# Performance work log

Measured on AMD Instinct MI355X. Metric: run time of the kernel, lower is better.

Reference implementation:

```python
import jax, jax.numpy as jnp
import numpy as np

CONF_THRESH = 0.05      # confidence_threshold
IOU_THRESH = 0.15       # nms_iou_threshold
MAX_PER_CLASS = 550     # max_detection_per_class
MAX_TOTAL = 1100        # max_detection
NEG = -1e9              # sentinel for suppressed / below-threshold scores


def _to_corners(b):
    # convert_to_min_max_corner: (cx, cy, w, h) -> (x1, y1, x2, y2)
    xy, wh = b[..., :2], b[..., 2:4]
    return jnp.concatenate([xy - wh * 0.5, xy + wh * 0.5], axis=-1)


def _area(b):
    return jnp.clip(b[..., 2] - b[..., 0], 0.0) * jnp.clip(b[..., 3] - b[..., 1], 0.0)


def _iou_one_many(box, boxes):
    # box: [4], boxes: [N,4] in corner format
    lt = jnp.maximum(box[:2], boxes[:, :2])
    rb = jnp.minimum(box[2:], boxes[:, 2:])
    wh = jnp.clip(rb - lt, 0.0)
    inter = wh[:, 0] * wh[:, 1]
    union = _area(box) + _area(boxes) - inter
    return inter / jnp.maximum(union, 1e-8)


def _nms_single(boxes, scores):
    # Exact greedy hard-NMS for one (image, class): boxes [N,4], scores [N]
    s0 = jnp.where(scores > CONF_THRESH, scores, NEG)

    def step(s, _):
        i = jnp.argmax(s)
        sc = s[i]
        suppress = _iou_one_many(boxes[i], boxes) > IOU_THRESH
        ns = jnp.where(suppress, NEG, s).at[i].set(NEG)
        return ns, (i, sc)

    _, (sel_idx, sel_score) = jax.lax.scan(step, s0, None, length=MAX_PER_CLASS)
    return sel_idx, sel_score  # [K], [K]


def _decode(predictions):
    boxes = _to_corners(predictions[:, :, :4])          # [B,N,4]
    cls_probs = jax.nn.sigmoid(predictions[:, :, 4:])   # [B,N,C]
    scores = jnp.transpose(cls_probs, (0, 2, 1))        # [B,C,N]

    nms = jax.vmap(jax.vmap(_nms_single, in_axes=(None, 0)), in_axes=(0, 0))
    sel_idx, sel_score = nms(boxes, scores)             # [B,C,K]
    B, C, K = sel_score.shape

    gboxes = jnp.take_along_axis(boxes[:, None, :, :], sel_idx[..., None], axis=2)  # [B,C,K,4]
    classes = jnp.broadcast_to(jnp.arange(C, dtype=jnp.float32)[None, :, None], (B, C, K))

    fb = gboxes.reshape(B, C * K, 4)
    fs = sel_score.reshape(B, C * K)
    fc = classes.reshape(B, C * K)

    k = min(MAX_TOTAL, C * K)
    top_s, top_i = jax.lax.top_k(fs, k)                 # combined cross-class top-k
    tb = jnp.take_along_axis(fb, top_i[..., None], axis=1)
    tc = jnp.take_along_axis(fc, top_i, axis=1)

    valid = top_s > 0.5 * NEG                           # real detections have score in (conf, 1]
    nmsed_boxes = jnp.where(valid[..., None], tb, 0.0)
    nmsed_scores = jnp.where(valid, top_s, 0.0)
    nmsed_classes = jnp.where(valid, tc, 0.0)
    valid_detections = jnp.sum(valid, axis=1).astype(jnp.int32)
    return nmsed_boxes, nmsed_scores, nmsed_classes, valid_detections


def setup_inputs() -> dict:
    key = jax.random.key(0)
    k1, k2, k3 = jax.random.split(key, 3)
    B, N, C, IMG = 4, 49104, 2, 512.0
    u = jax.random.uniform(k1, (B, N, 4), dtype=jnp.float32)
    cxcy = u[..., :2] * IMG                  # centers within the image
    wh = 16.0 + u[..., 2:] * 128.0           # plausible anchor-ish sizes
    logits = jax.random.normal(k2, (B, N, C), dtype=jnp.float32) * 1.5 - 3.0
    predictions = jnp.concatenate([cxcy, wh, logits], axis=-1)  # [B,N,6]
    images = jax.random.uniform(k3, (B, 512, 512, 3), dtype=jnp.float32)
    return {"images": images, "predictions": predictions}


def reference(images, predictions):
    # images is accepted (as in the Keras layer) but unused by the math
    return _decode(predictions)
```

## Files before the change

kernel.cpp:

```cpp
#include <hip/hip_runtime.h>
#include <stdint.h>

#define NEGV    (-1000000000.0f)
#define CONF    0.05f
#define MAXSEL  550
#define CAP     32768
#define HEAD    1024
#define HW      (HEAD / 64)
#define NBINS   4096
#define BINBASE 0xC07F0000u
#define GCAP    3072
#define NSEG    64
#define TROUNDS 3

typedef unsigned long long u64;
typedef unsigned int u32;

__device__ __forceinline__ float areaf(float4 b) {
    return __fmul_rn(fmaxf(__fsub_rn(b.z, b.x), 0.0f), fmaxf(__fsub_rn(b.w, b.y), 0.0f));
}

__device__ __forceinline__ bool iou_gt2(float4 a, float aA, float4 b, float aB) {
    float ltx = fmaxf(a.x, b.x), lty = fmaxf(a.y, b.y);
    float rbx = fminf(a.z, b.z), rby = fminf(a.w, b.w);
    float wx = fmaxf(__fsub_rn(rbx, ltx), 0.0f);
    float wy = fmaxf(__fsub_rn(rby, lty), 0.0f);
    float inter = __fmul_rn(wx, wy);
    float uni = fmaxf(__fsub_rn(__fadd_rn(aA, aB), inter), 1e-8f);
    const double M = (double)0.15f + 0x1p-27;
    return (double)inter > M * (double)uni;
}

__device__ __forceinline__ u32 binof(u32 keyhi) {
    u32 bin = (keyhi - BINBASE) >> 14;
    return bin > (NBINS - 1) ? (NBINS - 1) : bin;
}

__global__ void k_decode(const float* __restrict__ pred, float4* __restrict__ boxes,
                         u32* __restrict__ hist, u32* __restrict__ llen,
                         u32* __restrict__ S_arr, u32* __restrict__ Sold,
                         int BN, int NBC) {
    int t = blockIdx.x * 256 + threadIdx.x;
    if (t < 2 * NBC * NBINS) hist[t] = 0;
    if (t < 2 * NBC) llen[t] = 0;
    if (t < NBC) { S_arr[t] = 0; Sold[t] = 0; }
    if (t >= BN) return;
    const float* p = pred + (size_t)t * 6;
    float cx = p[0], cy = p[1], w = p[2], h = p[3];
    float hw = __fmul_rn(w, 0.5f), hh = __fmul_rn(h, 0.5f);
    float4 b;
    b.x = __fsub_rn(cx, hw);
    b.y = __fsub_rn(cy, hh);
    b.z = __fadd_rn(cx, hw);
    b.w = __fadd_rn(cy, hh);
    boxes[t] = b;
}

__global__ __launch_bounds__(256) void k_hist(const float* __restrict__ pred,
                                              u32* __restrict__ hist,
                                              u64* __restrict__ L0,
                                              u32* __restrict__ llen0,
                                              int Nn, int Cc, int TIL) {
    int bt = blockIdx.x;
    int tile = bt % TIL, bc = bt / TIL;
    int b = bc / Cc, c = bc % Cc;
    int n = tile * 256 + threadIdx.x;
    bool p = false; u32 hi = 0;
    if (n < Nn) {
        float lg = pred[((size_t)b * Nn + n) * 6 + 4 + c];
        float sc = __fdiv_rn(1.0f, __fadd_rn(1.0f, expf(-lg)));
        if (sc > CONF) {
            p = true;
            hi = ~__float_as_uint(sc);
            atomicAdd(&hist[bc * NBINS + binof(hi)], 1u);
        }
    }
    u64 bal = __ballot(p);
    __shared__ u32 wb[4]; __shared__ u32 base;
    int lane = threadIdx.x & 63, wv = threadIdx.x >> 6;
    if (lane == 0) wb[wv] = (u32)__popcll(bal);
    __syncthreads();
    if (threadIdx.x == 0) {
        u32 run = 0;
        for (int q = 0; q < 4; ++q) { u32 v = wb[q]; wb[q] = run; run += v; }
        base = run ? atomicAdd(&llen0[bc], run) : 0u;
    }
    __syncthreads();
    if (p) {
        u32 pos = base + wb[wv] + (u32)__popcll(bal & ((1ull << lane) - 1ull));
        if (pos < CAP)
            L0[(size_t)bc * CAP + pos] = ((u64)hi << 32) | (u32)n;
    }
}

__global__ __launch_bounds__(1024) void k_headsort(const u64* __restrict__ list,
                                                   const u32* __restrict__ llen_cur,
                                                   const u32* __restrict__ hc,
                                                   u32* __restrict__ hn,
                                                   u32* __restrict__ ln,
                                                   const float4* __restrict__ boxes,
                                                   const u32* __restrict__ S_arr,
                                                   u64* __restrict__ headkey,
                                                   float4* __restrict__ headbox,
                                                   float* __restrict__ headarea,
                                                   u32* __restrict__ hl_arr,
                                                   u64* __restrict__ hmax_arr,
                                                   int Nn, int Cc) {
    int bc = blockIdx.x, b = bc / Cc;
    int tid = threadIdx.x, lane = tid & 63, wv = tid >> 6;
    __shared__ u64 buf[4096];
    __shared__ u32 gcnt;
    __shared__ int s_t;
    for (int i = tid; i < NBINS; i += 1024) hn[bc * NBINS + i] = 0;
    if (tid == 0) { ln[bc] = 0; gcnt = 0; }
    __syncthreads();
    if ((int)S_arr[bc] >= MAXSEL) { if (tid == 0) hl_arr[bc] = 0; return; }
    int len = (int)llen_cur[bc]; if (len > CAP) len = CAP;
    if (wv == 0) {
        if (lane == 0) s_t = -1;
        const u32* h = hc + bc * NBINS;
        int base = lane * 64;
        u32 s = 0;
        for (int i = 0; i < 64; ++i) s += h[base + i];
        u32 p = s;
        for (int d = 1; d < 64; d <<= 1) { u32 o = __shfl_up(p, d); if (lane >= d) p += o; }
        u32 total = __shfl(p, 63);
        u32 K = total < HEAD ? total : HEAD;
        if (K > 0) {
            u64 bal = __ballot(p >= K);
            int tl = (int)__builtin_ctzll(bal);
            if (lane == tl) {
                u32 cum = p - s;
                for (int i = 0; i < 64; ++i) {
                    cum += h[base + i];
                    if (cum >= K) {
                        s_t = (cum <= GCAP) ? (base + i) : (base + i - 1);
                        break;
                    }
                }
            }
        }
    }
    __syncthreads();
    int t = s_t;
    if (t >= 0) {
        const u64* src = list + (size_t)bc * CAP;
        for (int i = tid; i < len; i += 1024) {
            u64 key = src[i];
            if ((int)binof((u32)(key >> 32)) <= t) {
                u32 pos = atomicAdd(&gcnt, 1u);
                if (pos < GCAP) buf[pos] = key;
            }
        }
    }
    __syncthreads();
    int g = (int)gcnt; if (g > GCAP) g = GCAP;
    int SN = 1; while (SN < g) SN <<= 1;
    for (int i = g + tid; i < SN; i += 1024) buf[i] = ~0ull;
    __syncthreads();
    for (int k = 2; k <= SN; k <<= 1) {
        for (int j = k >> 1; j > 0; j >>= 1) {
            for (int idx = tid; idx < SN / 2; idx += 1024) {
                int i = ((idx & ~(j - 1)) << 1) | (idx & (j - 1));
                int q = i | j;
                bool up = ((i & k) == 0);
                u64 x = buf[i], y = buf[q];
                if ((x > y) == up) { buf[i] = y; buf[q] = x; }
            }
            __syncthreads();
        }
    }
    int hl = g < HEAD ? g : HEAD;
    if (tid == 0) { hl_arr[bc] = (u32)hl; hmax_arr[bc] = hl > 0 ? buf[hl - 1] : 0ull; }
    for (int i = tid; i < hl; i += 1024) {
        u64 key = buf[i];
        headkey[bc * HEAD + i] = key;
        float4 bx = boxes[(size_t)b * Nn + (u32)key];
        headbox[bc * HEAD + i] = bx;
        headarea[bc * HEAD + i] = areaf(bx);
    }
}

__global__ __launch_bounds__(256) void k_premask(const float4* __restrict__ headbox,
                                                 const float* __restrict__ headarea,
                                                 const u32* __restrict__ hl_arr,
                                                 u64* __restrict__ masks) {
    int blk = blockIdx.x, bc = blk >> 4, rb = blk & 15;
    int hl = (int)hl_arr[bc];
    if (hl <= 0) return;
    __shared__ float4 chB[HEAD];
    __shared__ float  chA[HEAD];
    for (int i = threadIdx.x; i < hl; i += 256) {
        chB[i] = headbox[bc * HEAD + i];
        chA[i] = headarea[bc * HEAD + i];
    }
    __syncthreads();
    int r = (rb << 6) + (threadIdx.x & 63);
    int part = threadIdx.x >> 6;
    if (r >= hl) return;
    float4 a = chB[r]; float aA = chA[r];
    u64* row = masks + ((size_t)bc * HEAD + r) * HW;
    for (int w = part * 4; w < part * 4 + 4; ++w) {
        u64 bits = 0;
        int cb = w << 6;
        int j1 = hl - cb; if (j1 > 64) j1 = 64;
        int j0 = (cb > r) ? 0 : (r + 1 - cb);
        for (int j = j0; j < j1; ++j)
            if (iou_gt2(a, aA, chB[cb + j], chA[cb + j])) bits |= (1ull << j);
        row[w] = bits;
    }
}

__global__ __launch_bounds__(1024) void k_chain(const u64* __restrict__ headkey,
                                                const u32* __restrict__ hl_arr,
                                                const u64* __restrict__ masks,
                                                const float4* __restrict__ headbox,
                                                const float* __restrict__ headarea,
                                                u32* __restrict__ sel_n,
                                                float* __restrict__ sel_s,
                                                float4* __restrict__ selb_g,
                                                float* __restrict__ sela_g,
                                                u32* __restrict__ S_arr,
                                                u32* __restrict__ Sold) {
    int bc = blockIdx.x;
    int tid = threadIdx.x, lane = tid & 63;
    __shared__ u64 mrow[HEAD * HW];
    __shared__ u64 kky[HEAD];
    __shared__ u32 selidx[MAXSEL];
    __shared__ int s_S;
    int S0 = (int)S_arr[bc];
    if (tid == 0) Sold[bc] = (u32)S0;
    int hl = (int)hl_arr[bc];
    if (hl <= 0 || S0 >= MAXSEL) return;
    const u64* gm = masks + (size_t)bc * HEAD * HW;
    for (int i = tid; i < hl * HW; i += 1024) mrow[i] = gm[i];
    for (int i = tid; i < hl; i += 1024) kky[i] = headkey[bc * HEAD + i];
    __syncthreads();
    if (tid < 64) {
        u64 rem = ~0ull;
        if (lane < HW) {
            int lo = lane << 6;
            rem = (hl >= lo + 64) ? 0ull : (hl <= lo ? ~0ull : ~((1ull << (hl - lo)) - 1ull));
        }
        int S = S0;
        while (S < MAXSEL) {
            bool av = (lane < HW) && (rem != ~0ull);
            u64 bal = __ballot(av);
            if (!bal) break;
            int w0 = (int)__builtin_ctzll(bal);
            u64 nz = __shfl((u64)(~rem), w0);
            int kz = (int)__builtin_ctzll(nz);
            int i = (w0 << 6) + kz;
            if (lane == 0) selidx[S] = (u32)i;
            if (lane < HW) rem |= mrow[i * HW + lane];
            if (lane == w0) rem |= (1ull << kz);
            ++S;
        }
        if (lane == 0) { s_S = S; S_arr[bc] = (u32)S; }
    }
    __syncthreads();
    int S = s_S;
    for (int s = S0 + tid; s < S; s += 1024) {
        u32 i = selidx[s];
        u64 k64 = kky[i];
        sel_n[bc * MAXSEL + s] = (u32)k64;
        sel_s[bc * MAXSEL + s] = __uint_as_float(~(u32)(k64 >> 32));
        selb_g[bc * MAXSEL + s] = headbox[bc * HEAD + i];
        sela_g[bc * MAXSEL + s] = headarea[bc * HEAD + i];
    }
}

__global__ __launch_bounds__(256) void k_mark(const float4* __restrict__ boxes,
                                              const u64* __restrict__ Lc,
                                              const u32* __restrict__ llen_c,
                                              const float4* __restrict__ selb_g,
                                              const float* __restrict__ sela_g,
                                              const u32* __restrict__ S_arr,
                                              const u32* __restrict__ Sold,
                                              const u64* __restrict__ hmax_arr,
                                              const u32* __restrict__ hl_arr,
                                              u64* __restrict__ Ln,
                                              u32* __restrict__ llen_n,
                                              u32* __restrict__ hist_n,
                                              int Nn, int Cc) {
    int blk = blockIdx.x, bc = blk / NSEG, seg = blk % NSEG;
    int tid = threadIdx.x, lane = tid & 63, wv = tid >> 6;
    int b = bc / Cc;
    int S0 = (int)Sold[bc], S1 = (int)S_arr[bc];
    if (S1 >= MAXSEL) return;
    int len = (int)llen_c[bc]; if (len > CAP) len = CAP;
    if (len <= 0) return;
    int ns = S1 - S0;
    u64 hmax = ((int)hl_arr[bc] > 0) ? hmax_arr[bc] : 0ull;
    __shared__ float4 sb[MAXSEL];
    __shared__ float  sa[MAXSEL];
    for (int s = tid; s < ns; s += 256) {
        sb[s] = selb_g[bc * MAXSEL + S0 + s];
        sa[s] = sela_g[bc * MAXSEL + S0 + s];
    }
    __syncthreads();
    __shared__ u32 wb[4]; __shared__ u32 base;
    int chunk = (len + NSEG - 1) / NSEG;
    int lo = seg * chunk, hi2 = lo + chunk; if (hi2 > len) hi2 = len;
    const u64* src = Lc + (size_t)bc * CAP;
    u64* dst = Ln + (size_t)bc * CAP;
    for (int st = lo; st < hi2; st += 256) {
        int i = st + tid;
        bool alive = i < hi2; u64 key = 0;
        if (alive) {
            key = src[i];
            if (key <= hmax) alive = false;
            else {
                float4 bx = boxes[(size_t)b * Nn + (u32)key];
                float aA = areaf(bx);
                for (int s = 0; s < ns; ++s)
                    if (iou_gt2(bx, aA, sb[s], sa[s])) { alive = false; break; }
            }
        }
        u64 bal = __ballot(alive);
        if (lane == 0) wb[wv] = (u32)__popcll(bal);
        __syncthreads();
        if (tid == 0) {
            u32 run = 0;
            for (int q = 0; q < 4; ++q) { u32 v = wb[q]; wb[q] = run; run += v; }
            base = run ? atomicAdd(&llen_n[bc], run) : 0u;
        }
        __syncthreads();
        if (alive) {
            u32 pos = base + wb[wv] + (u32)__popcll(bal & ((1ull << lane) - 1ull));
            if (pos < CAP) dst[pos] = key;
            atomicAdd(&hist_n[bc * NBINS + binof((u32)(key >> 32))], 1u);
        }
        __syncthreads();
    }
}

__global__ __launch_bounds__(1024) void k_final(const u32* __restrict__ selcnt,
                                                const u32* __restrict__ sel_n,
                                                const float* __restrict__ sel_s,
                                                const float4* __restrict__ boxes,
                                                float* __restrict__ out,
                                                int Nn, int Cc, int Bb) {
    int b = blockIdx.x, tid = threadIdx.x;
    const int TOT = MAXSEL * 2;
    __shared__ u64 sk[2048];
    u32 c0 = selcnt[b * Cc + 0];
    u32 c1 = selcnt[b * Cc + 1];
    for (int t = tid; t < 2048; t += 1024) {
        u64 key;
        if (t < TOT) {
            int c = t / MAXSEL, k2 = t % MAXSEL;
            u32 cc = (c == 0) ? c0 : c1;
            float sc = (k2 < (int)cc) ? sel_s[(size_t)(b * Cc + c) * MAXSEL + k2] : NEGV;
            u32 u = __float_as_uint(sc);
            u32 ord = (u & 0x80000000u) ? ~u : (u | 0x80000000u);
            key = (((u64)(~ord)) << 32) | (u32)t;
        } else {
            key = ~0ull;
        }
        sk[t] = key;
    }
    __syncthreads();
    for (int k = 2; k <= 2048; k <<= 1) {
        for (int j = k >> 1; j > 0; j >>= 1) {
            int idx = tid;
            int i = ((idx & ~(j - 1)) << 1) | (idx & (j - 1));
            int p = i | j;
            bool up = ((i & k) == 0);
            u64 x = sk[i], y = sk[p];
            if ((x > y) == up) { sk[i] = y; sk[p] = x; }
            __syncthreads();
        }
    }
    int off_scores = Bb * TOT * 4;
    int off_classes = off_scores + Bb * TOT;
    int off_valid = off_classes + Bb * TOT;
    for (int r = tid; r < TOT; r += 1024) {
        u64 key = sk[r];
        u32 flat = (u32)(key & 0xffffffffull);
        u32 hi = (u32)(key >> 32);
        u32 ord = ~hi;
        float sc = (ord & 0x80000000u) ? __uint_as_float(ord & 0x7fffffffu)
                                       : __uint_as_float(~ord);
        bool valid = sc > -5.0e8f;
        int c = (int)(flat / MAXSEL), k2 = (int)(flat % MAXSEL);
        float4 bxv = make_float4(0.f, 0.f, 0.f, 0.f);
        float so = 0.f, co = 0.f;
        if (valid) {
            u32 n = sel_n[(size_t)(b * Cc + c) * MAXSEL + k2];
            bxv = boxes[(size_t)b * Nn + n];
            so = sc;
            co = (float)c;
        }
        ((float4*)out)[b * TOT + r] = bxv;
        out[off_scores + b * TOT + r] = so;
        out[off_classes + b * TOT + r] = co;
    }
    if (tid == 0) out[off_valid + b] = (float)(c0 + c1);
}

extern "C" void kernel_launch(void* const* d_in, const int* in_sizes, int n_in,
                              void* d_out, int out_size, void* d_ws, size_t ws_size,
                              hipStream_t stream) {
    const float* pred = (const float*)d_in[1];
    float* out = (float*)d_out;
    int Bb = out_size / 6601;
    int Nn = in_sizes[1] / (6 * Bb);
    const int Cc = 2;
    if (Bb <= 0 || Nn <= 0) return;
    int NBC = Bb * Cc;
    int TIL = (Nn + 255) / 256;

    char* ws = (char*)d_ws;
    size_t off = 0;
    auto alloc = [&](size_t bytes) { void* p = ws + off; off = (off + bytes + 255) & ~(size_t)255; return p; };
    float4* boxes   = (float4*)alloc((size_t)Bb * Nn * 16);
    u64* L0         = (u64*)alloc((size_t)NBC * CAP * 8);
    u64* L1         = (u64*)alloc((size_t)NBC * CAP * 8);
    u32* hist       = (u32*)alloc(2 * (size_t)NBC * NBINS * 4);
    u32* llen       = (u32*)alloc(2 * NBC * 4);
    u64* headkey    = (u64*)alloc((size_t)NBC * HEAD * 8);
    float4* headbox = (float4*)alloc((size_t)NBC * HEAD * 16);
    float* headarea = (float*)alloc((size_t)NBC * HEAD * 4);
    u32* hl_arr     = (u32*)alloc(NBC * 4);
    u64* hmax_arr   = (u64*)alloc(NBC * 8);
    u32* sel_n      = (u32*)alloc((size_t)NBC * MAXSEL * 4);
    float* sel_s    = (float*)alloc((size_t)NBC * MAXSEL * 4);
    float4* selb_g  = (float4*)alloc((size_t)NBC * MAXSEL * 16);
    float* sela_g   = (float*)alloc((size_t)NBC * MAXSEL * 4);
    u32* S_arr      = (u32*)alloc(NBC * 4);
    u32* Sold       = (u32*)alloc(NBC * 4);
    u64* masks      = (u64*)alloc((size_t)NBC * HEAD * HW * 8);
    if (off > ws_size) return;

    int BN = Bb * Nn;
    k_decode<<<(BN + 255) / 256, 256, 0, stream>>>(pred, boxes, hist, llen, S_arr, Sold, BN, NBC);
    k_hist<<<NBC * TIL, 256, 0, stream>>>(pred, hist, L0, llen, Nn, Cc, TIL);

    for (int r = 0; r < TROUNDS; ++r) {
        int cur = r & 1, nxt = (r + 1) & 1;
        u64* Lc = cur ? L1 : L0;
        u64* Ln = nxt ? L1 : L0;
        u32* lc = llen + cur * NBC;
        u32* ln = llen + nxt * NBC;
        u32* hc = hist + (size_t)cur * NBC * NBINS;
        u32* hn = hist + (size_t)nxt * NBC * NBINS;
        k_headsort<<<NBC, 1024, 0, stream>>>(Lc, lc, hc, hn, ln, boxes, S_arr,
                                             headkey, headbox, headarea, hl_arr, hmax_arr, Nn, Cc);
        k_premask<<<NBC * 16, 256, 0, stream>>>(headbox, headarea, hl_arr, masks);
        k_chain<<<NBC, 1024, 0, stream>>>(headkey, hl_arr, masks, headbox, headarea,
                                          sel_n, sel_s, selb_g, sela_g, S_arr, Sold);
        if (r + 1 < TROUNDS)
            k_mark<<<NBC * NSEG, 256, 0, stream>>>(boxes, Lc, lc, selb_g, sela_g, S_arr, Sold,
                                                   hmax_arr, hl_arr, Ln, ln, hn, Nn, Cc);
    }
    k_final<<<Bb, 1024, 0, stream>>>(S_arr, sel_n, sel_s, boxes, out, Nn, Cc, Bb);
}
```

Before: 359.2 us.

## Fuse decode with histogram build and fold IoU mask into headsort

Merges the box-decode and per-class histogram/list-building kernels into one pass that reads each prediction row once and handles both classes. Zeroing of hist/llen/S counters moves to a single memset, and the separate premask kernel is folded into headsort, so each thread computes its whole mask row from shared memory. This cuts the launch count per round and avoids rereading head boxes from global memory. The trade-off is that the mask computation now runs on only NBC blocks instead of NBC*16, which lowers parallelism, and headsort uses more shared memory.

```diff
diff --git a/kernel.cpp b/kernel.cpp
--- a/kernel.cpp
+++ b/kernel.cpp
@@ -36,60 +36,60 @@
     return bin > (NBINS - 1) ? (NBINS - 1) : bin;
 }
 
-__global__ void k_decode(const float* __restrict__ pred, float4* __restrict__ boxes,
-                         u32* __restrict__ hist, u32* __restrict__ llen,
-                         u32* __restrict__ S_arr, u32* __restrict__ Sold,
-                         int BN, int NBC) {
-    int t = blockIdx.x * 256 + threadIdx.x;
-    if (t < 2 * NBC * NBINS) hist[t] = 0;
-    if (t < 2 * NBC) llen[t] = 0;
-    if (t < NBC) { S_arr[t] = 0; Sold[t] = 0; }
-    if (t >= BN) return;
-    const float* p = pred + (size_t)t * 6;
-    float cx = p[0], cy = p[1], w = p[2], h = p[3];
-    float hw = __fmul_rn(w, 0.5f), hh = __fmul_rn(h, 0.5f);
-    float4 b;
-    b.x = __fsub_rn(cx, hw);
-    b.y = __fsub_rn(cy, hh);
-    b.z = __fadd_rn(cx, hw);
-    b.w = __fadd_rn(cy, hh);
-    boxes[t] = b;
-}
-
-__global__ __launch_bounds__(256) void k_hist(const float* __restrict__ pred,
-                                              u32* __restrict__ hist,
-                                              u64* __restrict__ L0,
-                                              u32* __restrict__ llen0,
-                                              int Nn, int Cc, int TIL) {
-    int bt = blockIdx.x;
-    int tile = bt % TIL, bc = bt / TIL;
-    int b = bc / Cc, c = bc % Cc;
-    int n = tile * 256 + threadIdx.x;
-    bool p = false; u32 hi = 0;
-    if (n < Nn) {
-        float lg = pred[((size_t)b * Nn + n) * 6 + 4 + c];
-        float sc = __fdiv_rn(1.0f, __fadd_rn(1.0f, expf(-lg)));
-        if (sc > CONF) {
-            p = true;
-            hi = ~__float_as_uint(sc);
-            atomicAdd(&hist[bc * NBINS + binof(hi)], 1u);
-        }
-    }
-    u64 bal = __ballot(p);
-    __shared__ u32 wb[4]; __shared__ u32 base;
-    int lane = threadIdx.x & 63, wv = threadIdx.x >> 6;
-    if (lane == 0) wb[wv] = (u32)__popcll(bal);
-    __syncthreads();
-    if (threadIdx.x == 0) {
-        u32 run = 0;
-        for (int q = 0; q < 4; ++q) { u32 v = wb[q]; wb[q] = run; run += v; }
-        base = run ? atomicAdd(&llen0[bc], run) : 0u;
-    }
-    __syncthreads();
-    if (p) {
-        u32 pos = base + wb[wv] + (u32)__popcll(bal & ((1ull << lane) - 1ull));
-        if (pos < CAP)
-            L0[(size_t)bc * CAP + pos] = ((u64)hi << 32) | (u32)n;
+__global__ __launch_bounds__(256) void k_build(const float* __restrict__ pred,
+                                               float4* __restrict__ boxes,
+                                               u32* __restrict__ hist,
+                                               u64* __restrict__ L0,
+                                               u32* __restrict__ llen0,
+                                               int Nn, int Cc, int TIL) {
+    int blk = blockIdx.x;
+    int tile = blk % TIL, b = blk / TIL;
+    int tid = threadIdx.x, lane = tid & 63, wv = tid >> 6;
+    int n = tile * 256 + tid;
+    bool inb = n < Nn;
+    float lg0 = 0.f, lg1 = 0.f;
+    if (inb) {
+        size_t base = ((size_t)b * Nn + n) * 6;
+        const float2* pp = (const float2*)(pred + base);
+        float2 r0 = pp[0], r1 = pp[1], r2 = pp[2];
+        float cx = r0.x, cy = r0.y, w = r1.x, h = r1.y;
+        float hw = __fmul_rn(w, 0.5f), hh = __fmul_rn(h, 0.5f);
+        float4 bx;
+        bx.x = __fsub_rn(cx, hw);
+        bx.y = __fsub_rn(cy, hh);
+        bx.z = __fadd_rn(cx, hw);
+        bx.w = __fadd_rn(cy, hh);
+        boxes[(size_t)b * Nn + n] = bx;
+        lg0 = r2.x; lg1 = r2.y;
+    }
+    __shared__ u32 wb[4]; __shared__ u32 sbase;
+    for (int c = 0; c < Cc; ++c) {
+        int bc = b * Cc + c;
+        bool p = false; u32 hi = 0;
+        if (inb) {
+            float lg = (c == 0) ? lg0 : lg1;
+            float sc = __fdiv_rn(1.0f, __fadd_rn(1.0f, expf(-lg)));
+            if (sc > CONF) {
+                p = true;
+                hi = ~__float_as_uint(sc);
+                atomicAdd(&hist[bc * NBINS + binof(hi)], 1u);
+            }
+        }
+        u64 bal = __ballot(p);
+        if (lane == 0) wb[wv] = (u32)__popcll(bal);
+        __syncthreads();
+        if (tid == 0) {
+            u32 run = 0;
+            for (int q = 0; q < 4; ++q) { u32 v = wb[q]; wb[q] = run; run += v; }
+            sbase = run ? atomicAdd(&llen0[bc], run) : 0u;
+        }
+        __syncthreads();
+        if (p) {
+            u32 pos = sbase + wb[wv] + (u32)__popcll(bal & ((1ull << lane) - 1ull));
+            if (pos < CAP)
+                L0[(size_t)bc * CAP + pos] = ((u64)hi << 32) | (u32)n;
+        }
+        __syncthreads();
     }
 }
 
@@ -105,10 +105,13 @@
                                                    float* __restrict__ headarea,
                                                    u32* __restrict__ hl_arr,
                                                    u64* __restrict__ hmax_arr,
+                                                   u64* __restrict__ masks,
                                                    int Nn, int Cc) {
     int bc = blockIdx.x, b = bc / Cc;
     int tid = threadIdx.x, lane = tid & 63, wv = tid >> 6;
     __shared__ u64 buf[4096];
+    __shared__ float4 chB[HEAD];
+    __shared__ float  chA[HEAD];
     __shared__ u32 gcnt;
     __shared__ int s_t;
     for (int i = tid; i < NBINS; i += 1024) hn[bc * NBINS + i] = 0;
@@ -178,36 +181,22 @@
         float4 bx = boxes[(size_t)b * Nn + (u32)key];
         headbox[bc * HEAD + i] = bx;
         headarea[bc * HEAD + i] = areaf(bx);
-    }
-}
-
-__global__ __launch_bounds__(256) void k_premask(const float4* __restrict__ headbox,
-                                                 const float* __restrict__ headarea,
-                                                 const u32* __restrict__ hl_arr,
-                                                 u64* __restrict__ masks) {
-    int blk = blockIdx.x, bc = blk >> 4, rb = blk & 15;
-    int hl = (int)hl_arr[bc];
-    if (hl <= 0) return;
-    __shared__ float4 chB[HEAD];
-    __shared__ float  chA[HEAD];
-    for (int i = threadIdx.x; i < hl; i += 256) {
-        chB[i] = headbox[bc * HEAD + i];
-        chA[i] = headarea[bc * HEAD + i];
-    }
-    __syncthreads();
-    int r = (rb << 6) + (threadIdx.x & 63);
-    int part = threadIdx.x >> 6;
-    if (r >= hl) return;
-    float4 a = chB[r]; float aA = chA[r];
-    u64* row = masks + ((size_t)bc * HEAD + r) * HW;
-    for (int w = part * 4; w < part * 4 + 4; ++w) {
-        u64 bits = 0;
-        int cb = w << 6;
-        int j1 = hl - cb; if (j1 > 64) j1 = 64;
-        int j0 = (cb > r) ? 0 : (r + 1 - cb);
-        for (int j = j0; j < j1; ++j)
-            if (iou_gt2(a, aA, chB[cb + j], chA[cb + j])) bits |= (1ull << j);
-        row[w] = bits;
+        chB[i] = bx;
+        chA[i] = areaf(bx);
+    }
+    __syncthreads();
+    if (tid < hl) {
+        float4 a = chB[tid]; float aA = chA[tid];
+        u64* row = masks + ((size_t)bc * HEAD + tid) * HW;
+        for (int w = 0; w < HW; ++w) {
+            u64 bits = 0;
+            int cb = w << 6;
+            int j1 = hl - cb; if (j1 > 64) j1 = 64;
+            int j0 = (cb > tid) ? 0 : (tid + 1 - cb);
+            for (int j = j0; j < j1; ++j)
+                if (iou_gt2(a, aA, chB[cb + j], chA[cb + j])) bits |= (1ull << j);
+            row[w] = bits;
+        }
     }
 }
 
@@ -417,8 +406,6 @@
     float4* boxes   = (float4*)alloc((size_t)Bb * Nn * 16);
     u64* L0         = (u64*)alloc((size_t)NBC * CAP * 8);
     u64* L1         = (u64*)alloc((size_t)NBC * CAP * 8);
-    u32* hist       = (u32*)alloc(2 * (size_t)NBC * NBINS * 4);
-    u32* llen       = (u32*)alloc(2 * NBC * 4);
     u64* headkey    = (u64*)alloc((size_t)NBC * HEAD * 8);
     float4* headbox = (float4*)alloc((size_t)NBC * HEAD * 16);
     float* headarea = (float*)alloc((size_t)NBC * HEAD * 4);
@@ -428,14 +415,17 @@
     float* sel_s    = (float*)alloc((size_t)NBC * MAXSEL * 4);
     float4* selb_g  = (float4*)alloc((size_t)NBC * MAXSEL * 16);
     float* sela_g   = (float*)alloc((size_t)NBC * MAXSEL * 4);
+    u64* masks      = (u64*)alloc((size_t)NBC * HEAD * HW * 8);
+    size_t zoff = off;
+    u32* hist       = (u32*)alloc(2 * (size_t)NBC * NBINS * 4);
+    u32* llen       = (u32*)alloc(2 * NBC * 4);
     u32* S_arr      = (u32*)alloc(NBC * 4);
     u32* Sold       = (u32*)alloc(NBC * 4);
-    u64* masks      = (u64*)alloc((size_t)NBC * HEAD * HW * 8);
+    size_t zbytes = off - zoff;
     if (off > ws_size) return;
 
-    int BN = Bb * Nn;
-    k_decode<<<(BN + 255) / 256, 256, 0, stream>>>(pred, boxes, hist, llen, S_arr, Sold, BN, NBC);
-    k_hist<<<NBC * TIL, 256, 0, stream>>>(pred, hist, L0, llen, Nn, Cc, TIL);
+    hipMemsetAsync(ws + zoff, 0, zbytes, stream);
+    k_build<<<Bb * TIL, 256, 0, stream>>>(pred, boxes, hist, L0, llen, Nn, Cc, TIL);
 
     for (int r = 0; r < TROUNDS; ++r) {
         int cur = r & 1, nxt = (r + 1) & 1;
@@ -446,8 +436,8 @@
         u32* hc = hist + (size_t)cur * NBC * NBINS;
         u32* hn = hist + (size_t)nxt * NBC * NBINS;
         k_headsort<<<NBC, 1024, 0, stream>>>(Lc, lc, hc, hn, ln, boxes, S_arr,
-                                             headkey, headbox, headarea, hl_arr, hmax_arr, Nn, Cc);
-        k_premask<<<NBC * 16, 256, 0, stream>>>(headbox, headarea, hl_arr, masks);
+                                             headkey, headbox, headarea, hl_arr, hmax_arr,
+                                             masks, Nn, Cc);
         k_chain<<<NBC, 1024, 0, stream>>>(headkey, hl_arr, masks, headbox, headarea,
                                           sel_n, sel_s, selb_g, sela_g, S_arr, Sold);
         if (r + 1 < TROUNDS)
```

Result: slower. 511.9 us (+42.5%).
